# Kernel tuning notes

Measured on AMD Instinct MI355X. Metric: run time of the kernel, lower is better.

## Reference

```python
import jax, jax.numpy as jnp
import numpy as np

H = 16  # num_heads
D = 64  # depth per head


def setup_inputs() -> dict:
    key = jax.random.key(0)
    ks = jax.random.split(key, 9)
    hd = H * D
    s = 1.0 / np.sqrt(hd)
    return {
        "x": jax.random.normal(ks[0], (2, 2048, hd), dtype=jnp.float32),
        "wq_w": jax.random.normal(ks[1], (hd, hd), dtype=jnp.float32) * s,
        "wq_b": jnp.zeros((hd,), dtype=jnp.float32),
        "wk_w": jax.random.normal(ks[2], (hd, hd), dtype=jnp.float32) * s,
        "wk_b": jnp.zeros((hd,), dtype=jnp.float32),
        "wv_w": jax.random.normal(ks[3], (hd, hd), dtype=jnp.float32) * s,
        "wv_b": jnp.zeros((hd,), dtype=jnp.float32),
        "fc_w": jax.random.normal(ks[4], (hd, hd), dtype=jnp.float32) * s,
        "fc_b": jnp.zeros((hd,), dtype=jnp.float32),
    }


def reference(x, wq_w, wq_b, wk_w, wk_b, wv_w, wv_b, fc_w, fc_b):
    B, S, HD = x.shape
    # Linear layers (torch Linear: y = x @ W^T + b)
    q = x @ wq_w.T + wq_b
    k = x @ wk_w.T + wk_b
    v = x @ wv_w.T + wv_b
    # split heads -> [B, H, S, D]
    split = lambda t: t.reshape(B, S, H, D).transpose(0, 2, 1, 3)
    q, k, v = split(q), split(k), split(v)
    scale = 1.0 / jnp.sqrt(jnp.float32(D))
    logits = jnp.einsum("bhqd,bhkd->bhqk", q, k) * scale
    attn = jax.nn.softmax(logits, axis=-1)
    out = jnp.einsum("bhqk,bhkd->bhqd", attn, v)
    out = out.transpose(0, 2, 1, 3).reshape(B, S, HD)
    return out @ fc_w.T + fc_b
```

## Files before the change

kernel.cpp:

```cpp
#include <hip/hip_runtime.h>
#include <hip/hip_bf16.h>

typedef __hip_bfloat16 bf16;
typedef __attribute__((ext_vector_type(8))) short bf16x8;
typedef __attribute__((ext_vector_type(4))) float f32x4;
typedef __attribute__((ext_vector_type(16))) float f32x16;

static constexpr int SEQ = 2048;
static constexpr int HDIM = 1024;
static constexpr int NH = 16;
static constexpr int DH = 64;

__device__ __forceinline__ f32x4 mfma16(bf16x8 a, bf16x8 b, f32x4 c) {
  return __builtin_amdgcn_mfma_f32_16x16x32_bf16(a, b, c, 0, 0, 0);
}
__device__ __forceinline__ f32x16 mfma32(bf16x8 a, bf16x8 b, f32x16 c) {
  return __builtin_amdgcn_mfma_f32_32x32x16_bf16(a, b, c, 0, 0, 0);
}

__device__ __forceinline__ void gload_lds16(const bf16* g, bf16* l) {
  __builtin_amdgcn_global_load_lds(
      (const __attribute__((address_space(1))) void*)g,
      (__attribute__((address_space(3))) void*)l, 16, 0, 0);
}

__device__ __forceinline__ unsigned packbf(float a, float b) {
  unsigned short ua = __builtin_bit_cast(unsigned short, __float2bfloat16(a));
  unsigned short ub = __builtin_bit_cast(unsigned short, __float2bfloat16(b));
  return (unsigned)ua | ((unsigned)ub << 16);
}

__global__ __launch_bounds__(256) void cvt_bf16(const float* __restrict__ in,
                                                bf16* __restrict__ out, int n4) {
  int i = blockIdx.x * blockDim.x + threadIdx.x;
  if (i >= n4) return;
  float4 v = reinterpret_cast<const float4*>(in)[i];
  bf16 t[4] = {__float2bfloat16(v.x), __float2bfloat16(v.y),
               __float2bfloat16(v.z), __float2bfloat16(v.w)};
  reinterpret_cast<ushort4*>(out)[i] = *reinterpret_cast<ushort4*>(t);
}

__device__ __forceinline__ void gemm_core(const bf16* __restrict__ A,
                                          const bf16* __restrict__ W,
                                          int m0, int n0, int K,
                                          f32x4 (&acc)[4][4],
                                          bf16* As, bf16* Bs) {
  const int tid = threadIdx.x;
  const int w = tid >> 6, lane = tid & 63;
  const int wr = w >> 1, wc = w & 1;
  const int lr = lane & 15, lk = (lane >> 4) * 8;
  const int srow = lane >> 2, scol = (lane & 3) * 8;

  for (int kt = 0; kt < K; kt += 32) {
#pragma unroll
    for (int j = 0; j < 2; ++j) {
      int cidx = w * 2 + j;
      int r = cidx * 16 + srow;
      gload_lds16(A + (size_t)(m0 + r) * K + kt + scol, As + cidx * 512);
      gload_lds16(W + (size_t)(n0 + r) * K + kt + scol, Bs + cidx * 512);
    }
    __syncthreads();
    bf16x8 af[4], bw[4];
#pragma unroll
    for (int i = 0; i < 4; ++i)
      af[i] = *reinterpret_cast<const bf16x8*>(As + (wr * 64 + i * 16 + lr) * 32 + lk);
#pragma unroll
    for (int i = 0; i < 4; ++i)
      bw[i] = *reinterpret_cast<const bf16x8*>(Bs + (wc * 64 + i * 16 + lr) * 32 + lk);
#pragma unroll
    for (int r = 0; r < 4; ++r)
#pragma unroll
      for (int c = 0; c < 4; ++c)
        acc[r][c] = mfma16(af[r], bw[c], acc[r][c]);
    __syncthreads();
  }
}

__global__ __launch_bounds__(256)
void qkv_gemm(const bf16* __restrict__ xb,
              const bf16* __restrict__ wq, const bf16* __restrict__ wk,
              const bf16* __restrict__ wv,
              const float* __restrict__ bq, const float* __restrict__ bk,
              const float* __restrict__ bv,
              bf16* __restrict__ qd, bf16* __restrict__ kd, bf16* __restrict__ vT) {
  __shared__ bf16 As[128 * 32], Bs[128 * 32];
  const int z = blockIdx.z;
  const bf16* W = (z == 0) ? wq : (z == 1) ? wk : wv;
  const float* bias = (z == 0) ? bq : (z == 1) ? bk : bv;
  const float scale = (z == 0) ? 0.125f : 1.0f;
  const int m0 = blockIdx.y * 128, n0 = blockIdx.x * 128;
  f32x4 acc[4][4] = {};
  gemm_core(xb, W, m0, n0, HDIM, acc, As, Bs);

  const int tid = threadIdx.x, w = tid >> 6, lane = tid & 63;
  const int wr = w >> 1, wc = w & 1;
  const int lr = lane & 15, rg = (lane >> 4) * 4;
#pragma unroll
  for (int r = 0; r < 4; ++r)
#pragma unroll
    for (int c = 0; c < 4; ++c) {
      int n = n0 + wc * 64 + c * 16 + lr;
      int h = n >> 6, d = n & 63;
      float bz = bias[n];
#pragma unroll
      for (int q = 0; q < 4; ++q) {
        int m = m0 + wr * 64 + r * 16 + rg + q;
        int b = m >> 11, s = m & 2047;
        bf16 val = __float2bfloat16((acc[r][c][q] + bz) * scale);
        if (z == 2)
          vT[(((size_t)(b * NH + h) * DH + d) << 11) + s] = val;
        else {
          bf16* dst = (z == 0) ? qd : kd;
          dst[(((size_t)(b * NH + h) * SEQ + s) << 6) + d] = val;
        }
      }
    }
}

__global__ __launch_bounds__(256)
void attn_kernel(const bf16* __restrict__ Q, const bf16* __restrict__ K,
                 const bf16* __restrict__ vT, bf16* __restrict__ AO) {
  __shared__ float als[4][32];
  const int lane = threadIdx.x & 63;
  const int wv = threadIdx.x >> 6;
  const int l31 = lane & 31;
  const int hi = lane >> 5;
  const int bh = blockIdx.y;
  const int b = bh >> 4, h = bh & 15;
  const int q0 = blockIdx.x * 128 + wv * 32;

  const bf16* Qh = Q + (size_t)bh * SEQ * DH;
  const bf16* Kh = K + (size_t)bh * SEQ * DH;
  const bf16* Vh = vT + (size_t)bh * DH * SEQ;

  bf16x8 qf[4];
#pragma unroll
  for (int s = 0; s < 4; ++s)
    qf[s] = *reinterpret_cast<const bf16x8*>(
        Qh + (size_t)(q0 + l31) * DH + s * 16 + hi * 8);

  f32x16 o0 = {}, o1 = {};
  float m = -1e30f, l = 0.f;

  for (int kt = 0; kt < SEQ; kt += 32) {
    f32x16 sacc = {};
#pragma unroll
    for (int s = 0; s < 4; ++s) {
      bf16x8 kf = *reinterpret_cast<const bf16x8*>(
          Kh + (size_t)(kt + l31) * DH + s * 16 + hi * 8);
      sacc = mfma32(kf, qf[s], sacc);
    }
    bf16x8 vf[2][2];
#pragma unroll
    for (int kh = 0; kh < 2; ++kh)
#pragma unroll
      for (int t = 0; t < 2; ++t)
        vf[kh][t] = *reinterpret_cast<const bf16x8*>(
            Vh + (size_t)(t * 32 + l31) * SEQ + kt + kh * 16 + hi * 8);

    float pmax = sacc[0];
#pragma unroll
    for (int i = 1; i < 16; ++i) pmax = fmaxf(pmax, sacc[i]);
    pmax = fmaxf(pmax, __shfl_xor(pmax, 32));

    if (__any(pmax > m + 8.0f)) {
      float mn = fmaxf(m, pmax);
      float al = exp2f((m - mn) * 1.442695041f);
      m = mn; l *= al;
      if (lane < 32) als[wv][l31] = al;
      __builtin_amdgcn_wave_barrier();
#pragma unroll
      for (int r = 0; r < 16; ++r) {
        float a = als[wv][(r & 3) + 8 * (r >> 2) + 4 * hi];
        o0[r] *= a; o1[r] *= a;
      }
      __builtin_amdgcn_wave_barrier();
    }

    const float mc = m * 1.442695041f;
    float p[16];
    float ps = 0.f;
#pragma unroll
    for (int i = 0; i < 16; ++i) {
      p[i] = exp2f(sacc[i] * 1.442695041f - mc);
      ps += p[i];
    }
    ps += __shfl_xor(ps, 32);
    l += ps;

    unsigned w[4][2], sw[4][2];
#pragma unroll
    for (int g = 0; g < 4; ++g) {
      w[g][0] = packbf(p[4 * g + 0], p[4 * g + 1]);
      w[g][1] = packbf(p[4 * g + 2], p[4 * g + 3]);
      sw[g][0] = __shfl_xor(w[g][0], 32);
      sw[g][1] = __shfl_xor(w[g][1], 32);
    }
#pragma unroll
    for (int kh = 0; kh < 2; ++kh) {
      union { unsigned u[4]; bf16x8 v; } fa;
      fa.u[0] = hi ? sw[2 * kh + 1][0] : w[2 * kh][0];
      fa.u[1] = hi ? sw[2 * kh + 1][1] : w[2 * kh][1];
      fa.u[2] = hi ? w[2 * kh + 1][0] : sw[2 * kh][0];
      fa.u[3] = hi ? w[2 * kh + 1][1] : sw[2 * kh][1];
      o0 = mfma32(fa.v, vf[kh][0], o0);
      o1 = mfma32(fa.v, vf[kh][1], o1);
    }
  }

  if (lane < 32) als[wv][l31] = l;
  __builtin_amdgcn_wave_barrier();
#pragma unroll
  for (int r = 0; r < 16; ++r) {
    int q = (r & 3) + 8 * (r >> 2) + 4 * hi;
    float inv = 1.0f / als[wv][q];
    size_t row = (size_t)(b * SEQ + q0 + q) * HDIM + h * DH;
    AO[row + l31] = __float2bfloat16(o0[r] * inv);
    AO[row + 32 + l31] = __float2bfloat16(o1[r] * inv);
  }
}

__global__ __launch_bounds__(256)
void fc_gemm(const bf16* __restrict__ A, const bf16* __restrict__ W,
             const float* __restrict__ bias, float* __restrict__ out) {
  __shared__ bf16 As[128 * 32], Bs[128 * 32];
  const int m0 = blockIdx.y * 128, n0 = blockIdx.x * 128;
  f32x4 acc[4][4] = {};
  gemm_core(A, W, m0, n0, HDIM, acc, As, Bs);

  const int tid = threadIdx.x, w = tid >> 6, lane = tid & 63;
  const int wr = w >> 1, wc = w & 1;
  const int lr = lane & 15, rg = (lane >> 4) * 4;
#pragma unroll
  for (int r = 0; r < 4; ++r)
#pragma unroll
    for (int c = 0; c < 4; ++c) {
      int n = n0 + wc * 64 + c * 16 + lr;
      float bz = bias[n];
#pragma unroll
      for (int q = 0; q < 4; ++q) {
        int m = m0 + wr * 64 + r * 16 + rg + q;
        out[(size_t)m * HDIM + n] = acc[r][c][q] + bz;
      }
    }
}

extern "C" void kernel_launch(void* const* d_in, const int* in_sizes, int n_in,
                              void* d_out, int out_size, void* d_ws, size_t ws_size,
                              hipStream_t stream) {
  (void)in_sizes; (void)n_in; (void)out_size; (void)ws_size;
  const float* x  = (const float*)d_in[0];
  const float* wq = (const float*)d_in[1];
  const float* bq = (const float*)d_in[2];
  const float* wk = (const float*)d_in[3];
  const float* bk = (const float*)d_in[4];
  const float* wv = (const float*)d_in[5];
  const float* bv = (const float*)d_in[6];
  const float* wf = (const float*)d_in[7];
  const float* bf_ = (const float*)d_in[8];
  float* out = (float*)d_out;

  char* ws = (char*)d_ws;
  bf16* xb  = (bf16*)(ws);
  bf16* wqb = (bf16*)(ws + (8u << 20));
  bf16* wkb = (bf16*)(ws + (10u << 20));
  bf16* wvb = (bf16*)(ws + (12u << 20));
  bf16* wfb = (bf16*)(ws + (14u << 20));
  bf16* qd  = (bf16*)(ws + (16u << 20));
  bf16* kd  = (bf16*)(ws + (24u << 20));
  bf16* vT  = (bf16*)(ws + (32u << 20));
  bf16* ao  = (bf16*)(ws + (40u << 20));

  cvt_bf16<<<4096, 256, 0, stream>>>(x, xb, 1048576);
  cvt_bf16<<<1024, 256, 0, stream>>>(wq, wqb, 262144);
  cvt_bf16<<<1024, 256, 0, stream>>>(wk, wkb, 262144);
  cvt_bf16<<<1024, 256, 0, stream>>>(wv, wvb, 262144);
  cvt_bf16<<<1024, 256, 0, stream>>>(wf, wfb, 262144);

  qkv_gemm<<<dim3(8, 32, 3), 256, 0, stream>>>(xb, wqb, wkb, wvb, bq, bk, bv,
                                               qd, kd, vT);
  attn_kernel<<<dim3(16, 32), 256, 0, stream>>>(qd, kd, vT, ao);
  fc_gemm<<<dim3(8, 32), 256, 0, stream>>>(ao, wfb, bf_, out);
}
```

Before: 273.8 us.

## Split attention key range across two wave groups and fold log2e into Q scale

```diff
diff --git a/kernel.cpp b/kernel.cpp
--- a/kernel.cpp
+++ b/kernel.cpp
@@ -87,7 +87,7 @@
   const int z = blockIdx.z;
   const bf16* W = (z == 0) ? wq : (z == 1) ? wk : wv;
   const float* bias = (z == 0) ? bq : (z == 1) ? bk : bv;
-  const float scale = (z == 0) ? 0.125f : 1.0f;
+  const float scale = (z == 0) ? 0.18033688011f : 1.0f;
   const int m0 = blockIdx.y * 128, n0 = blockIdx.x * 128;
   f32x4 acc[4][4] = {};
   gemm_core(xb, W, m0, n0, HDIM, acc, As, Bs);
@@ -117,17 +117,22 @@
     }
 }
 
-__global__ __launch_bounds__(256)
+__global__ __launch_bounds__(512, 4)
 void attn_kernel(const bf16* __restrict__ Q, const bf16* __restrict__ K,
                  const bf16* __restrict__ vT, bf16* __restrict__ AO) {
-  __shared__ float als[4][32];
+  __shared__ float Olds[4][32][64];
+  __shared__ float mlds[4][32], llds[4][32];
+  __shared__ float als[8][32];
+  __shared__ float af1[4][32], af2[4][32], li[4][32];
+
   const int lane = threadIdx.x & 63;
   const int wv = threadIdx.x >> 6;
+  const int qw = wv & 3, kh = wv >> 2;
   const int l31 = lane & 31;
   const int hi = lane >> 5;
   const int bh = blockIdx.y;
   const int b = bh >> 4, h = bh & 15;
-  const int q0 = blockIdx.x * 128 + wv * 32;
+  const int q0 = blockIdx.x * 128 + qw * 32;
 
   const bf16* Qh = Q + (size_t)bh * SEQ * DH;
   const bf16* Kh = K + (size_t)bh * SEQ * DH;
@@ -142,7 +147,8 @@
   f32x16 o0 = {}, o1 = {};
   float m = -1e30f, l = 0.f;
 
-  for (int kt = 0; kt < SEQ; kt += 32) {
+  const int k_lo = kh << 10, k_hi = k_lo + 1024;
+  for (int kt = k_lo; kt < k_hi; kt += 32) {
     f32x16 sacc = {};
 #pragma unroll
     for (int s = 0; s < 4; ++s) {
@@ -152,20 +158,23 @@
     }
     bf16x8 vf[2][2];
 #pragma unroll
-    for (int kh = 0; kh < 2; ++kh)
+    for (int kk = 0; kk < 2; ++kk)
 #pragma unroll
       for (int t = 0; t < 2; ++t)
-        vf[kh][t] = *reinterpret_cast<const bf16x8*>(
-            Vh + (size_t)(t * 32 + l31) * SEQ + kt + kh * 16 + hi * 8);
-
-    float pmax = sacc[0];
-#pragma unroll
-    for (int i = 1; i < 16; ++i) pmax = fmaxf(pmax, sacc[i]);
+        vf[kk][t] = *reinterpret_cast<const bf16x8*>(
+            Vh + (size_t)(t * 32 + l31) * SEQ + kt + kk * 16 + hi * 8);
+
+    float tm[8];
+#pragma unroll
+    for (int i = 0; i < 8; ++i) tm[i] = fmaxf(sacc[2 * i], sacc[2 * i + 1]);
+#pragma unroll
+    for (int i = 0; i < 4; ++i) tm[i] = fmaxf(tm[i], tm[i + 4]);
+    float pmax = fmaxf(fmaxf(tm[0], tm[1]), fmaxf(tm[2], tm[3]));
     pmax = fmaxf(pmax, __shfl_xor(pmax, 32));
 
-    if (__any(pmax > m + 8.0f)) {
+    if (__any(pmax > m + 11.5415603f)) {
       float mn = fmaxf(m, pmax);
-      float al = exp2f((m - mn) * 1.442695041f);
+      float al = exp2f(m - mn);
       m = mn; l *= al;
       if (lane < 32) als[wv][l31] = al;
       __builtin_amdgcn_wave_barrier();
@@ -177,14 +186,15 @@
       __builtin_amdgcn_wave_barrier();
     }
 
-    const float mc = m * 1.442695041f;
     float p[16];
-    float ps = 0.f;
-#pragma unroll
-    for (int i = 0; i < 16; ++i) {
-      p[i] = exp2f(sacc[i] * 1.442695041f - mc);
-      ps += p[i];
-    }
+#pragma unroll
+    for (int i = 0; i < 16; ++i) p[i] = exp2f(sacc[i] - m);
+    float ts[8];
+#pragma unroll
+    for (int i = 0; i < 8; ++i) ts[i] = p[2 * i] + p[2 * i + 1];
+#pragma unroll
+    for (int i = 0; i < 4; ++i) ts[i] = ts[i] + ts[i + 4];
+    float ps = (ts[0] + ts[1]) + (ts[2] + ts[3]);
     ps += __shfl_xor(ps, 32);
     l += ps;
 
@@ -197,26 +207,44 @@
       sw[g][1] = __shfl_xor(w[g][1], 32);
     }
 #pragma unroll
-    for (int kh = 0; kh < 2; ++kh) {
+    for (int kk = 0; kk < 2; ++kk) {
       union { unsigned u[4]; bf16x8 v; } fa;
-      fa.u[0] = hi ? sw[2 * kh + 1][0] : w[2 * kh][0];
-      fa.u[1] = hi ? sw[2 * kh + 1][1] : w[2 * kh][1];
-      fa.u[2] = hi ? w[2 * kh + 1][0] : sw[2 * kh][0];
-      fa.u[3] = hi ? w[2 * kh + 1][1] : sw[2 * kh][1];
-      o0 = mfma32(fa.v, vf[kh][0], o0);
-      o1 = mfma32(fa.v, vf[kh][1], o1);
+      fa.u[0] = hi ? sw[2 * kk + 1][0] : w[2 * kk][0];
+      fa.u[1] = hi ? sw[2 * kk + 1][1] : w[2 * kk][1];
+      fa.u[2] = hi ? w[2 * kk + 1][0] : sw[2 * kk][0];
+      fa.u[3] = hi ? w[2 * kk + 1][1] : sw[2 * kk][1];
+      o0 = mfma32(fa.v, vf[kk][0], o0);
+      o1 = mfma32(fa.v, vf[kk][1], o1);
     }
   }
 
-  if (lane < 32) als[wv][l31] = l;
-  __builtin_amdgcn_wave_barrier();
-#pragma unroll
-  for (int r = 0; r < 16; ++r) {
-    int q = (r & 3) + 8 * (r >> 2) + 4 * hi;
-    float inv = 1.0f / als[wv][q];
-    size_t row = (size_t)(b * SEQ + q0 + q) * HDIM + h * DH;
-    AO[row + l31] = __float2bfloat16(o0[r] * inv);
-    AO[row + 32 + l31] = __float2bfloat16(o1[r] * inv);
+  if (kh == 1) {
+    if (lane < 32) { mlds[qw][l31] = m; llds[qw][l31] = l; }
+#pragma unroll
+    for (int r = 0; r < 16; ++r) {
+      int q = (r & 3) + 8 * (r >> 2) + 4 * hi;
+      Olds[qw][q][l31] = o0[r];
+      Olds[qw][q][32 + l31] = o1[r];
+    }
+  }
+  __syncthreads();
+  if (kh == 0) {
+    float m2 = mlds[qw][l31], l2 = llds[qw][l31];
+    float mn = fmaxf(m, m2);
+    float a1 = exp2f(m - mn), a2 = exp2f(m2 - mn);
+    float inv = 1.0f / (l * a1 + l2 * a2);
+    if (lane < 32) { af1[qw][l31] = a1; af2[qw][l31] = a2; li[qw][l31] = inv; }
+    __builtin_amdgcn_wave_barrier();
+#pragma unroll
+    for (int r = 0; r < 16; ++r) {
+      int q = (r & 3) + 8 * (r >> 2) + 4 * hi;
+      float s1 = af1[qw][q], s2 = af2[qw][q], iv = li[qw][q];
+      size_t row = (size_t)(b * SEQ + q0 + q) * HDIM + h * DH;
+      AO[row + l31] =
+          __float2bfloat16((o0[r] * s1 + Olds[qw][q][l31] * s2) * iv);
+      AO[row + 32 + l31] =
+          __float2bfloat16((o1[r] * s1 + Olds[qw][q][32 + l31] * s2) * iv);
+    }
   }
 }
 
@@ -279,6 +307,6 @@
 
   qkv_gemm<<<dim3(8, 32, 3), 256, 0, stream>>>(xb, wqb, wkb, wvb, bq, bk, bv,
                                                qd, kd, vT);
-  attn_kernel<<<dim3(16, 32), 256, 0, stream>>>(qd, kd, vT, ao);
+  attn_kernel<<<dim3(16, 32), 512, 0, stream>>>(qd, kd, vT, ao);
   fc_gemm<<<dim3(8, 32), 256, 0, stream>>>(ao, wfb, bf_, out);
 }
```

Result: no change. 274.1 us (+0.1%).
